# Optimization experiments

Measured on AMD Instinct MI355X. Metric: run time of the kernel, lower is better.

The kernel has to match this reference:

```python
import jax, jax.numpy as jnp
import numpy as np

NUM_FRAMES = 8
NUM_CLASSES = 40
INNER_TH = 0.5
MIN_WH = 0.05
SUPPRESS = 1e9


def _xyxy_to_cxcywh(b):
    x1, y1, x2, y2 = b[..., 0], b[..., 1], b[..., 2], b[..., 3]
    return jnp.stack([(x1 + x2) * 0.5, (y1 + y2) * 0.5, x2 - x1, y2 - y1], -1)


def setup_inputs() -> dict:
    key = jax.random.key(0)
    k1, k2, k3, k4, k5 = jax.random.split(key, 5)
    B, N, T = 4, 20, NUM_FRAMES
    H = W = 160
    # valid xyxy boxes: centers in [0.1,0.9], wh in [0.02,0.3]
    c = jax.random.uniform(k1, (B, N, T, 2), minval=0.1, maxval=0.9)
    wh = jax.random.uniform(k2, (B, N, T, 2), minval=0.02, maxval=0.3)
    gt_boxes = jnp.concatenate([c - wh / 2, c + wh / 2], -1).astype(jnp.float32)
    gt_labels = jax.random.randint(k3, (B, N), 0, NUM_CLASSES)
    ids = jax.random.randint(k4, (B, N, T), 0, 100)
    drop = jax.random.bernoulli(k5, 0.1, (B, N, T))
    gt_ids = jnp.where(drop, -1, ids)  # -1 => instance absent in that frame
    ys, xs = jnp.meshgrid(jnp.arange(H), jnp.arange(W), indexing='ij')
    ref_points = jnp.stack([(xs.reshape(-1) + 0.5) / W, (ys.reshape(-1) + 0.5) / H], -1).astype(jnp.float32)
    spatial_shapes = jnp.array([H, W], dtype=jnp.int32)
    return dict(gt_labels=gt_labels, gt_boxes=gt_boxes, gt_ids=gt_ids,
                ref_points=ref_points, spatial_shapes=spatial_shapes)


def _match_frame(dist_t, ids_t, labels, valid):
    # dist_t [N,P], ids_t [N], labels [N], valid [N]; sequential suppression over n
    N, P = dist_t.shape
    arangeP = jnp.arange(P)
    arangeC = jnp.arange(NUM_CLASSES)

    def step(carry, n):
        d_all, ml, md, mi = carry
        d = d_all[n]                                   # [P]
        act = valid[n] & (ids_t[n] != -1)
        inner = d < INNER_TH
        # if no inner point, claim just the single closest point
        pos = jnp.where(inner.any(), inner, arangeP == jnp.argmin(d)) & act
        lab = labels[n]
        score = 1.0 - 2.0 * jnp.clip(d, 0.0, INNER_TH)
        ml = jnp.where(pos, lab, ml)
        md = jnp.where(pos[:, None] & (arangeC == lab)[None, :], score[:, None], md)
        mi = jnp.where(pos, ids_t[n], mi)
        d_all = jnp.where(pos[None, :], SUPPRESS, d_all)  # suppress claimed points for all gts
        return (d_all, ml, md, mi), None

    init = (dist_t,
            jnp.full((P,), -1, jnp.int32),
            jnp.zeros((P, NUM_CLASSES), dist_t.dtype),
            jnp.full((P,), -1, jnp.int32))
    (_, ml, md, mi), _ = jax.lax.scan(step, init, jnp.arange(N))
    return ml, md, mi


def reference(gt_labels, gt_boxes, gt_ids, ref_points, spatial_shapes):
    B, N, T, _ = gt_boxes.shape
    boxes_c = _xyxy_to_cxcywh(gt_boxes)                 # [B,N,T,4]
    area = (boxes_c[..., 2] * boxes_c[..., 3]).mean(-1)  # [B,N] mean area over frames
    order = jnp.argsort(area, axis=1)                   # process small instances first
    boxes_c = jnp.take_along_axis(boxes_c, order[:, :, None, None], axis=1)
    labels = jnp.take_along_axis(gt_labels.astype(jnp.int32), order, axis=1)
    ids = jnp.take_along_axis(gt_ids.astype(jnp.int32), order[:, :, None], axis=1)
    valid = (boxes_c[..., 2:] > 0.0).all(-1).any(-1) & (labels >= 0)  # [B,N]
    # normalized center distance: [B,N,T,P]
    diff = (boxes_c[..., None, :2] - ref_points[None, None, None, :, :]) / jnp.clip(boxes_c[..., None, 2:], MIN_WH)
    dist = jnp.sum(diff ** 2, -1)
    f = jax.vmap(jax.vmap(_match_frame, in_axes=(1, 1, None, None)), in_axes=(0, 0, 0, 0))
    ml, md, mi = f(dist, ids, labels, valid)            # [B,T,P], [B,T,P,C], [B,T,P]
    return ml, md, mi
```

## Files before the change

kernel.cpp:

```cpp
#include <hip/hip_runtime.h>

#define BB   4
#define NGT  20
#define TT   8
#define PP   25600
#define CC   40
#define TPB  256
#define SUPP 1e9f
#define INNER_TH 0.5f
#define FILLB 224

#define PK_CLAIM  1u
#define PK_LAB_SH 1
#define PK_ID_SH  7
#define PK_MDV    (1u << 14)
#define PK_MDC_SH 15
#define PK_MDN_SH 21

__device__ inline unsigned long long shfl_down_u64(unsigned long long v, int off) {
    unsigned lo = (unsigned)v, hi = (unsigned)(v >> 32);
    lo = __shfl_down(lo, off, 64);
    hi = __shfl_down(hi, off, 64);
    return ((unsigned long long)hi << 32) | (unsigned long long)lo;
}

__device__ inline float4 make_geo(const float* __restrict__ gt_boxes, int b, int n, int t) {
    const float* bx = gt_boxes + ((size_t)(b * NGT + n) * TT + t) * 4;
    float x1 = bx[0], y1 = bx[1], x2 = bx[2], y2 = bx[3];
    float4 g;
    g.x = __fmul_rn(__fadd_rn(x1, x2), 0.5f);
    g.y = __fmul_rn(__fadd_rn(y1, y2), 0.5f);
    g.z = fmaxf(__fsub_rn(x2, x1), 0.05f);
    g.w = fmaxf(__fsub_rn(y2, y1), 0.05f);
    return g;
}

__device__ inline float point_dist(int px, int py, float4 g) {
    float rxv = __fdiv_rn((float)px + 0.5f, 160.0f);
    float ryv = __fdiv_rn((float)py + 0.5f, 160.0f);
    float dx = __fdiv_rn(__fsub_rn(g.x, rxv), g.z);
    float dy = __fdiv_rn(__fsub_rn(g.y, ryv), g.w);
    return __fadd_rn(__fmul_rn(dx, dx), __fmul_rn(dy, dy));
}

__global__ __launch_bounds__(TPB) void match_fill_kernel(
        const int*   __restrict__ gt_labels,
        const float* __restrict__ gt_boxes,
        const int*   __restrict__ gt_ids,
        unsigned* __restrict__ packs_g,
        uint4*    __restrict__ md4) {
    if (blockIdx.x >= BB * TT) {
        const int MD4 = BB * TT * PP * CC / 4;
        const int stride = FILLB * TPB;
        uint4 z = make_uint4(0u, 0u, 0u, 0u);
        for (int i = (blockIdx.x - BB * TT) * TPB + (int)threadIdx.x; i < MD4; i += stride)
            md4[i] = z;
        return;
    }

    int bt = blockIdx.x;
    int b  = bt >> 3;
    int t  = bt & 7;
    int tid = threadIdx.x;

    __shared__ unsigned s_pack[PP];
    __shared__ unsigned s_mask[160 * 5];
    __shared__ float  s_dxx[NGT * 160];
    __shared__ float  s_dyy[NGT * 160];
    __shared__ float  s_area[NGT];
    __shared__ int    s_valid[NGT];
    __shared__ int    s_order[NGT];
    __shared__ int    s_any[NGT];
    __shared__ float4 s_geo[NGT];
    __shared__ int4   s_meta[NGT];
    __shared__ int    s_actlist[NGT];
    __shared__ int    s_actcnt;
    __shared__ unsigned long long s_wave[TPB / 64];

    {
        uint4 z = make_uint4(0u, 0u, 0u, 0u);
        for (int i = tid; i < PP / 4; i += TPB) ((uint4*)s_pack)[i] = z;
        for (int i = tid; i < 160 * 5; i += TPB) s_mask[i] = 0u;
    }
    if (tid < NGT) {
        const float* bx = gt_boxes + (size_t)(b * NGT + tid) * TT * 4;
        float a[TT];
        int anyPos = 0;
        for (int f = 0; f < TT; f++) {
            float w = __fsub_rn(bx[f * 4 + 2], bx[f * 4 + 0]);
            float h = __fsub_rn(bx[f * 4 + 3], bx[f * 4 + 1]);
            a[f] = __fmul_rn(w, h);
            anyPos |= (w > 0.0f && h > 0.0f) ? 1 : 0;
        }
        float s = __fadd_rn(__fadd_rn(__fadd_rn(a[0], a[1]), __fadd_rn(a[2], a[3])),
                            __fadd_rn(__fadd_rn(a[4], a[5]), __fadd_rn(a[6], a[7])));
        s_area[tid]  = __fmul_rn(s, 0.125f);
        s_valid[tid] = (anyPos && gt_labels[b * NGT + tid] >= 0) ? 1 : 0;
        s_any[tid]   = 0;
    }
    __syncthreads();

    if (tid < NGT) {
        float an = s_area[tid];
        int r = 0;
        for (int m2 = 0; m2 < NGT; m2++) {
            float am = s_area[m2];
            r += (am < an || (am == an && m2 < tid)) ? 1 : 0;
        }
        s_order[r] = tid;
    }
    __syncthreads();

    if (tid < NGT) {
        int n   = s_order[tid];
        int src = b * NGT + n;
        s_geo[tid] = make_geo(gt_boxes, b, n, t);
        int id = gt_ids[src * TT + t];
        int4 mm;
        mm.x = gt_labels[src];
        mm.y = id;
        mm.z = (s_valid[n] && id != -1) ? 1 : 0;
        mm.w = n;
        s_meta[tid] = mm;
    }
    __syncthreads();
    if (tid == 0) {
        int c = 0;
        for (int k = 0; k < NGT; k++)
            if (s_meta[k].z) s_actlist[c++] = k;
        s_actcnt = c;
    }

    for (int i = tid; i < NGT * 320; i += TPB) {
        int slot = i / 320;
        int w    = i - slot * 320;
        float4 g = s_geo[slot];
        if (w < 160) {
            float rxv = __fdiv_rn((float)w + 0.5f, 160.0f);
            float dx  = __fdiv_rn(__fsub_rn(g.x, rxv), g.z);
            s_dxx[slot * 160 + w] = __fmul_rn(dx, dx);
        } else {
            int py = w - 160;
            float ryv = __fdiv_rn((float)py + 0.5f, 160.0f);
            float dy  = __fdiv_rn(__fsub_rn(g.y, ryv), g.w);
            s_dyy[slot * 160 + py] = __fmul_rn(dy, dy);
        }
    }
    __syncthreads();
    int actcnt = s_actcnt;

    for (int j = 0; j < actcnt; j++) {
        int slot = s_actlist[j];
        int4 m  = s_meta[slot];
        float4 g = s_geo[slot];
        const float* dxx = s_dxx + slot * 160;
        const float* dyy = s_dyy + slot * 160;

        float ex = __fmul_rn(g.z, 0.70711f);
        float ey = __fmul_rn(g.w, 0.70711f);
        int x0 = max(0,   (int)floorf((g.x - ex) * 160.0f - 0.5f) - 1);
        int x1 = min(159, (int)ceilf ((g.x + ex) * 160.0f - 0.5f) + 1);
        int y0 = max(0,   (int)floorf((g.y - ey) * 160.0f - 0.5f) - 1);
        int y1 = min(159, (int)ceilf ((g.y + ey) * 160.0f - 0.5f) + 1);
        int rw = x1 - x0 + 1;
        int M  = rw * (y1 - y0 + 1);

        unsigned base = PK_CLAIM | ((unsigned)m.x << PK_LAB_SH) |
                        ((unsigned)m.y << PK_ID_SH) | PK_MDV |
                        ((unsigned)m.x << PK_MDC_SH) |
                        ((unsigned)m.w << PK_MDN_SH);
        int found = 0;
        {
            int r  = tid / rw;
            int c  = tid - r * rw;
            int dr = TPB / rw;
            int dc = TPB - dr * rw;
            for (int i = tid; i < M; i += TPB) {
                int px = x0 + c;
                int py = y0 + r;
                int p  = py * 160 + px;
                if (!(s_pack[p] & PK_CLAIM)) {
                    float d = __fadd_rn(dxx[px], dyy[py]);
                    if (d < INNER_TH) {
                        s_pack[p] = base;
                        atomicOr(&s_mask[p >> 5], 1u << (p & 31));
                        found = 1;
                    }
                }
                c += dc; r += dr;
                if (c >= rw) { c -= rw; r++; }
            }
        }
        if (found) s_any[j] = 1;
        __syncthreads();

        if (!s_any[j]) {
            unsigned long long key = ~0ULL;
            if (tid < 160) {
                int y = tid;
                unsigned um[5];
#pragma unroll
                for (int w = 0; w < 5; w++) um[w] = ~s_mask[y * 5 + w];
                unsigned anyu = um[0] | um[1] | um[2] | um[3] | um[4];
                if (!anyu) {
                    if (y == 0)
                        key = ((unsigned long long)__float_as_uint(SUPP) << 32);
                } else {
                    float dyyv = dyy[y];
                    int xs = (int)floorf(__fsub_rn(__fmul_rn(g.x, 160.0f), 0.5f));
                    xs = min(max(xs, -2), 161);
                    float bd = 2e9f;
                    int   bx = -1;
#pragma unroll
                    for (int k2 = 0; k2 < 2; k2++) {
                        int x = xs + k2;
                        if (x >= 0 && x <= 159 && ((um[x >> 5] >> (x & 31)) & 1u)) {
                            float d2 = __fadd_rn(dxx[x], dyyv);
                            if (d2 < bd || (d2 == bd && x < bx)) { bd = d2; bx = x; }
                        }
                    }
                    {
                        int xq = min(xs - 1, 159);
                        int xL = -1;
                        if (xq >= 0) {
                            int w = xq >> 5;
                            unsigned mm = um[w] & (0xffffffffu >> (31 - (xq & 31)));
                            while (true) {
                                if (mm) { xL = (w << 5) + (31 - __clz(mm)); break; }
                                if (--w < 0) break;
                                mm = um[w];
                            }
                        }
                        if (xL >= 0) {
                            float dL = __fadd_rn(dxx[xL], dyyv);
                            while (xL > 0) {
                                int xq2 = xL - 1;
                                int w = xq2 >> 5;
                                unsigned mm = um[w] & (0xffffffffu >> (31 - (xq2 & 31)));
                                int x2 = -1;
                                while (true) {
                                    if (mm) { x2 = (w << 5) + (31 - __clz(mm)); break; }
                                    if (--w < 0) break;
                                    mm = um[w];
                                }
                                if (x2 < 0) break;
                                if (__fadd_rn(dxx[x2], dyyv) != dL) break;
                                xL = x2;
                            }
                            if (dL < bd || (dL == bd && xL < bx)) { bd = dL; bx = xL; }
                        }
                    }
                    {
                        int xq = max(xs + 2, 0);
                        int xR = -1;
                        if (xq <= 159) {
                            int w = xq >> 5;
                            unsigned mm = um[w] & (0xffffffffu << (xq & 31));
                            while (true) {
                                if (mm) { xR = (w << 5) + (__ffs(mm) - 1); break; }
                                if (++w > 4) break;
                                mm = um[w];
                            }
                        }
                        if (xR >= 0) {
                            float dR = __fadd_rn(dxx[xR], dyyv);
                            if (dR < bd || (dR == bd && xR < bx)) { bd = dR; bx = xR; }
                        }
                    }
                    if (bx >= 0) {
                        int p = y * 160 + bx;
                        key = ((unsigned long long)__float_as_uint(bd) << 32) |
                              (unsigned long long)(unsigned)p;
                    }
                }
            }
            unsigned long long v = key;
            for (int off = 32; off > 0; off >>= 1) {
                unsigned long long o = shfl_down_u64(v, off);
                v = (o < v) ? o : v;
            }
            int lane = tid & 63, wave = tid >> 6;
            if (lane == 0) s_wave[wave] = v;
            __syncthreads();
            if (tid == 0) {
                unsigned long long gmin = s_wave[0];
                for (int w = 1; w < TPB / 64; w++)
                    gmin = (s_wave[w] < gmin) ? s_wave[w] : gmin;
                float minv = __uint_as_float((unsigned)(gmin >> 32));
                int minp = (int)(unsigned)(gmin & 0xffffffffu);
                unsigned npk = PK_CLAIM | ((unsigned)m.x << PK_LAB_SH) |
                               ((unsigned)m.y << PK_ID_SH);
                if (minv < SUPP) {
                    s_pack[minp] = npk;
                } else {
                    unsigned old = s_pack[minp];
                    unsigned mdbits = old & (PK_MDV | (63u << PK_MDC_SH) | (31u << PK_MDN_SH));
                    if ((old & PK_MDV) &&
                        ((old >> PK_MDC_SH) & 63u) == (unsigned)m.x) mdbits = 0u;
                    s_pack[minp] = npk | mdbits;
                }
                s_mask[minp >> 5] |= 1u << (minp & 31);
            }
            __syncthreads();
        }
    }

    __syncthreads();
    uint4* dst = (uint4*)(packs_g + (size_t)bt * PP);
    for (int i = tid; i < PP / 4; i += TPB) dst[i] = ((const uint4*)s_pack)[i];
}

__global__ __launch_bounds__(256) void scatter_kernel(
        const unsigned* __restrict__ packs,
        const float*    __restrict__ gt_boxes,
        float* __restrict__ out) {
    const int    ML = BB * TT * PP;
    const size_t MD = (size_t)BB * TT * PP * CC;
    int f = blockIdx.x * 256 + threadIdx.x;
    uint4 pk4 = ((const uint4*)packs)[f];

    float4 vml, vmi;
    vml.x = (pk4.x & PK_CLAIM) ? (float)((pk4.x >> PK_LAB_SH) & 63u) : -1.0f;
    vml.y = (pk4.y & PK_CLAIM) ? (float)((pk4.y >> PK_LAB_SH) & 63u) : -1.0f;
    vml.z = (pk4.z & PK_CLAIM) ? (float)((pk4.z >> PK_LAB_SH) & 63u) : -1.0f;
    vml.w = (pk4.w & PK_CLAIM) ? (float)((pk4.w >> PK_LAB_SH) & 63u) : -1.0f;
    vmi.x = (pk4.x & PK_CLAIM) ? (float)((pk4.x >> PK_ID_SH) & 127u) : -1.0f;
    vmi.y = (pk4.y & PK_CLAIM) ? (float)((pk4.y >> PK_ID_SH) & 127u) : -1.0f;
    vmi.z = (pk4.z & PK_CLAIM) ? (float)((pk4.z >> PK_ID_SH) & 127u) : -1.0f;
    vmi.w = (pk4.w & PK_CLAIM) ? (float)((pk4.w >> PK_ID_SH) & 127u) : -1.0f;
    ((float4*)out)[f] = vml;
    ((float4*)(out + ML + MD))[f] = vmi;

    int pt0 = f << 2;
#pragma unroll
    for (int k = 0; k < 4; k++) {
        unsigned pk = (k == 0) ? pk4.x : (k == 1) ? pk4.y : (k == 2) ? pk4.z : pk4.w;
        if (pk & PK_MDV) {
            int pt  = pt0 + k;
            int cls = (int)((pk >> PK_MDC_SH) & 63u);
            int n   = (int)((pk >> PK_MDN_SH) & 31u);
            int bt  = pt / PP;
            int p   = pt - bt * PP;
            int py  = p / 160;
            int px  = p - py * 160;
            float4 g = make_geo(gt_boxes, bt >> 3, n, bt & 7);
            float d  = point_dist(px, py, g);
            out[ML + (size_t)pt * CC + cls] = __fsub_rn(1.0f, __fmul_rn(2.0f, d));
        }
    }
}

extern "C" void kernel_launch(void* const* d_in, const int* in_sizes, int n_in,
                              void* d_out, int out_size, void* d_ws, size_t ws_size,
                              hipStream_t stream) {
    const int*   gt_labels = (const int*)d_in[0];
    const float* gt_boxes  = (const float*)d_in[1];
    const int*   gt_ids    = (const int*)d_in[2];

    unsigned* packs = (unsigned*)d_ws;
    float*    outf  = (float*)d_out;

    match_fill_kernel<<<BB * TT + FILLB, TPB, 0, stream>>>(
        gt_labels, gt_boxes, gt_ids, packs,
        (uint4*)(outf + BB * TT * PP));

    scatter_kernel<<<(BB * TT * PP / 4) / 256, 256, 0, stream>>>(packs, gt_boxes, outf);
}
```

Measured before the change: 181.5 us.

## Replace sequential inner-point claiming with parallel atomicMin ownership and fallback pass

The serial per-GT claim loop, which needed a barrier after every ground truth, becomes a single parallel pass. Each in-range point takes the smallest slot index that has it inside its threshold via shared atomicMin. Per-slot claim counts come from ballots, and the closest-point fallback runs only for slots with zero claims, rebuilding the claimed mask from byte owners. The block grows to 1024 threads, and the label/id outputs are written directly from the matching kernel with byte-sized owner codes. The scatter kernel then only writes the score entries, which removes the packed word round-trip but adds a fallback-suppression special case.

```diff
diff --git a/kernel.cpp b/kernel.cpp
--- a/kernel.cpp
+++ b/kernel.cpp
@@ -5,17 +5,12 @@
 #define TT   8
 #define PP   25600
 #define CC   40
-#define TPB  256
+#define TPB  1024
 #define SUPP 1e9f
 #define INNER_TH 0.5f
 #define FILLB 224
-
-#define PK_CLAIM  1u
-#define PK_LAB_SH 1
-#define PK_ID_SH  7
-#define PK_MDV    (1u << 14)
-#define PK_MDC_SH 15
-#define PK_MDN_SH 21
+#define NONEC 63u
+#define FBF   64u
 
 __device__ inline unsigned long long shfl_down_u64(unsigned long long v, int off) {
     unsigned lo = (unsigned)v, hi = (unsigned)(v >> 32);
@@ -47,8 +42,11 @@
         const int*   __restrict__ gt_labels,
         const float* __restrict__ gt_boxes,
         const int*   __restrict__ gt_ids,
-        unsigned* __restrict__ packs_g,
-        uint4*    __restrict__ md4) {
+        unsigned char* __restrict__ cand_ws,
+        int2*          __restrict__ meta_ws,
+        unsigned char* __restrict__ supp_ws,
+        float*         __restrict__ out,
+        uint4*         __restrict__ md4) {
     if (blockIdx.x >= BB * TT) {
         const int MD4 = BB * TT * PP * CC / 4;
         const int stride = FILLB * TPB;
@@ -61,26 +59,28 @@
     int bt = blockIdx.x;
     int b  = bt >> 3;
     int t  = bt & 7;
-    int tid = threadIdx.x;
-
-    __shared__ unsigned s_pack[PP];
-    __shared__ unsigned s_mask[160 * 5];
+    int tid  = threadIdx.x;
+    int lane = tid & 63;
+
+    __shared__ unsigned      s_cand[PP];
+    __shared__ unsigned char s_candb[PP];
+    __shared__ unsigned      s_mask[160 * 5];
     __shared__ float  s_dxx[NGT * 160];
     __shared__ float  s_dyy[NGT * 160];
     __shared__ float  s_area[NGT];
     __shared__ int    s_valid[NGT];
     __shared__ int    s_order[NGT];
-    __shared__ int    s_any[NGT];
     __shared__ float4 s_geo[NGT];
     __shared__ int4   s_meta[NGT];
     __shared__ int    s_actlist[NGT];
     __shared__ int    s_actcnt;
+    __shared__ int    s_count[NGT];
     __shared__ unsigned long long s_wave[TPB / 64];
+    __shared__ unsigned s_suppmd;
 
     {
-        uint4 z = make_uint4(0u, 0u, 0u, 0u);
-        for (int i = tid; i < PP / 4; i += TPB) ((uint4*)s_pack)[i] = z;
-        for (int i = tid; i < 160 * 5; i += TPB) s_mask[i] = 0u;
+        uint4 ini = make_uint4(NONEC, NONEC, NONEC, NONEC);
+        for (int i = tid; i < PP / 4; i += TPB) ((uint4*)s_cand)[i] = ini;
     }
     if (tid < NGT) {
         const float* bx = gt_boxes + (size_t)(b * NGT + tid) * TT * 4;
@@ -96,8 +96,9 @@
                             __fadd_rn(__fadd_rn(a[4], a[5]), __fadd_rn(a[6], a[7])));
         s_area[tid]  = __fmul_rn(s, 0.125f);
         s_valid[tid] = (anyPos && gt_labels[b * NGT + tid] >= 0) ? 1 : 0;
-        s_any[tid]   = 0;
-    }
+        s_count[tid] = 0;
+    }
+    if (tid == 0) s_suppmd = 255u;
     __syncthreads();
 
     if (tid < NGT) {
@@ -149,13 +150,11 @@
     __syncthreads();
     int actcnt = s_actcnt;
 
-    for (int j = 0; j < actcnt; j++) {
-        int slot = s_actlist[j];
-        int4 m  = s_meta[slot];
+    for (int jj = 0; jj < actcnt; jj++) {
+        int slot = s_actlist[jj];
         float4 g = s_geo[slot];
         const float* dxx = s_dxx + slot * 160;
         const float* dyy = s_dyy + slot * 160;
-
         float ex = __fmul_rn(g.z, 0.70711f);
         float ey = __fmul_rn(g.w, 0.70711f);
         int x0 = max(0,   (int)floorf((g.x - ex) * 160.0f - 0.5f) - 1);
@@ -164,188 +163,230 @@
         int y1 = min(159, (int)ceilf ((g.y + ey) * 160.0f - 0.5f) + 1);
         int rw = x1 - x0 + 1;
         int M  = rw * (y1 - y0 + 1);
-
-        unsigned base = PK_CLAIM | ((unsigned)m.x << PK_LAB_SH) |
-                        ((unsigned)m.y << PK_ID_SH) | PK_MDV |
-                        ((unsigned)m.x << PK_MDC_SH) |
-                        ((unsigned)m.w << PK_MDN_SH);
-        int found = 0;
-        {
-            int r  = tid / rw;
-            int c  = tid - r * rw;
-            int dr = TPB / rw;
-            int dc = TPB - dr * rw;
-            for (int i = tid; i < M; i += TPB) {
-                int px = x0 + c;
-                int py = y0 + r;
-                int p  = py * 160 + px;
-                if (!(s_pack[p] & PK_CLAIM)) {
-                    float d = __fadd_rn(dxx[px], dyy[py]);
-                    if (d < INNER_TH) {
-                        s_pack[p] = base;
-                        atomicOr(&s_mask[p >> 5], 1u << (p & 31));
-                        found = 1;
+        int r  = tid / rw;
+        int c  = tid - r * rw;
+        int dr = TPB / rw;
+        int dc = TPB - dr * rw;
+        for (int i = tid; i < M; i += TPB) {
+            int px = x0 + c;
+            int py = y0 + r;
+            float d = __fadd_rn(dxx[px], dyy[py]);
+            if (d < INNER_TH) atomicMin(&s_cand[py * 160 + px], (unsigned)slot);
+            c += dc; r += dr;
+            if (c >= rw) { c -= rw; r++; }
+        }
+    }
+    __syncthreads();
+
+    {
+        unsigned lcnt = 0;
+        for (int i = tid; i < PP; i += TPB) {
+            unsigned cc = s_cand[i];
+            s_candb[i] = (unsigned char)cc;
+            for (int k = 0; k < NGT; k++) {
+                unsigned long long bl = __ballot(cc == (unsigned)k);
+                if (lane == k) lcnt += (unsigned)__popcll(bl);
+            }
+        }
+        if (lane < NGT) atomicAdd(&s_count[lane], (int)lcnt);
+    }
+    __syncthreads();
+
+    for (int jj = 0; jj < actcnt; jj++) {
+        int slot = s_actlist[jj];
+        if (s_count[slot] != 0) continue;
+
+        int4 m  = s_meta[slot];
+        float4 g = s_geo[slot];
+        const float* dxx = s_dxx + slot * 160;
+        const float* dyy = s_dyy + slot * 160;
+
+        for (int w = tid; w < 160 * 5; w += TPB) {
+            const unsigned* cw = ((const unsigned*)s_candb) + (w << 3);
+            unsigned mb = 0u;
+#pragma unroll
+            for (int q = 0; q < 8; q++) {
+                unsigned v = cw[q];
+                mb |= (((v        & 63u) < (unsigned)slot) ? 1u : 0u) << (q * 4 + 0);
+                mb |= ((((v >> 8)  & 63u) < (unsigned)slot) ? 1u : 0u) << (q * 4 + 1);
+                mb |= ((((v >> 16) & 63u) < (unsigned)slot) ? 1u : 0u) << (q * 4 + 2);
+                mb |= ((((v >> 24) & 63u) < (unsigned)slot) ? 1u : 0u) << (q * 4 + 3);
+            }
+            s_mask[w] = mb;
+        }
+        __syncthreads();
+
+        unsigned long long key = ~0ULL;
+        if (tid < 160) {
+            int y = tid;
+            unsigned um[5];
+#pragma unroll
+            for (int w = 0; w < 5; w++) um[w] = ~s_mask[y * 5 + w];
+            unsigned anyu = um[0] | um[1] | um[2] | um[3] | um[4];
+            if (!anyu) {
+                if (y == 0)
+                    key = ((unsigned long long)__float_as_uint(SUPP) << 32);
+            } else {
+                float dyyv = dyy[y];
+                int xs = (int)floorf(__fsub_rn(__fmul_rn(g.x, 160.0f), 0.5f));
+                xs = min(max(xs, -2), 161);
+                float bd = 2e9f;
+                int   bx = -1;
+#pragma unroll
+                for (int k2 = 0; k2 < 2; k2++) {
+                    int x = xs + k2;
+                    if (x >= 0 && x <= 159 && ((um[x >> 5] >> (x & 31)) & 1u)) {
+                        float d2 = __fadd_rn(dxx[x], dyyv);
+                        if (d2 < bd || (d2 == bd && x < bx)) { bd = d2; bx = x; }
                     }
                 }
-                c += dc; r += dr;
-                if (c >= rw) { c -= rw; r++; }
-            }
-        }
-        if (found) s_any[j] = 1;
-        __syncthreads();
-
-        if (!s_any[j]) {
-            unsigned long long key = ~0ULL;
-            if (tid < 160) {
-                int y = tid;
-                unsigned um[5];
-#pragma unroll
-                for (int w = 0; w < 5; w++) um[w] = ~s_mask[y * 5 + w];
-                unsigned anyu = um[0] | um[1] | um[2] | um[3] | um[4];
-                if (!anyu) {
-                    if (y == 0)
-                        key = ((unsigned long long)__float_as_uint(SUPP) << 32);
-                } else {
-                    float dyyv = dyy[y];
-                    int xs = (int)floorf(__fsub_rn(__fmul_rn(g.x, 160.0f), 0.5f));
-                    xs = min(max(xs, -2), 161);
-                    float bd = 2e9f;
-                    int   bx = -1;
-#pragma unroll
-                    for (int k2 = 0; k2 < 2; k2++) {
-                        int x = xs + k2;
-                        if (x >= 0 && x <= 159 && ((um[x >> 5] >> (x & 31)) & 1u)) {
-                            float d2 = __fadd_rn(dxx[x], dyyv);
-                            if (d2 < bd || (d2 == bd && x < bx)) { bd = d2; bx = x; }
+                {
+                    int xq = min(xs - 1, 159);
+                    int xL = -1;
+                    if (xq >= 0) {
+                        int w = xq >> 5;
+                        unsigned mm = um[w] & (0xffffffffu >> (31 - (xq & 31)));
+                        while (true) {
+                            if (mm) { xL = (w << 5) + (31 - __clz(mm)); break; }
+                            if (--w < 0) break;
+                            mm = um[w];
                         }
                     }
-                    {
-                        int xq = min(xs - 1, 159);
-                        int xL = -1;
-                        if (xq >= 0) {
-                            int w = xq >> 5;
-                            unsigned mm = um[w] & (0xffffffffu >> (31 - (xq & 31)));
+                    if (xL >= 0) {
+                        float dL = __fadd_rn(dxx[xL], dyyv);
+                        while (xL > 0) {
+                            int xq2 = xL - 1;
+                            int w = xq2 >> 5;
+                            unsigned mm = um[w] & (0xffffffffu >> (31 - (xq2 & 31)));
+                            int x2 = -1;
                             while (true) {
-                                if (mm) { xL = (w << 5) + (31 - __clz(mm)); break; }
+                                if (mm) { x2 = (w << 5) + (31 - __clz(mm)); break; }
                                 if (--w < 0) break;
                                 mm = um[w];
                             }
+                            if (x2 < 0) break;
+                            if (__fadd_rn(dxx[x2], dyyv) != dL) break;
+                            xL = x2;
                         }
-                        if (xL >= 0) {
-                            float dL = __fadd_rn(dxx[xL], dyyv);
-                            while (xL > 0) {
-                                int xq2 = xL - 1;
-                                int w = xq2 >> 5;
-                                unsigned mm = um[w] & (0xffffffffu >> (31 - (xq2 & 31)));
-                                int x2 = -1;
-                                while (true) {
-                                    if (mm) { x2 = (w << 5) + (31 - __clz(mm)); break; }
-                                    if (--w < 0) break;
-                                    mm = um[w];
-                                }
-                                if (x2 < 0) break;
-                                if (__fadd_rn(dxx[x2], dyyv) != dL) break;
-                                xL = x2;
-                            }
-                            if (dL < bd || (dL == bd && xL < bx)) { bd = dL; bx = xL; }
+                        if (dL < bd || (dL == bd && xL < bx)) { bd = dL; bx = xL; }
+                    }
+                }
+                {
+                    int xq = max(xs + 2, 0);
+                    int xR = -1;
+                    if (xq <= 159) {
+                        int w = xq >> 5;
+                        unsigned mm = um[w] & (0xffffffffu << (xq & 31));
+                        while (true) {
+                            if (mm) { xR = (w << 5) + (__ffs(mm) - 1); break; }
+                            if (++w > 4) break;
+                            mm = um[w];
                         }
                     }
-                    {
-                        int xq = max(xs + 2, 0);
-                        int xR = -1;
-                        if (xq <= 159) {
-                            int w = xq >> 5;
-                            unsigned mm = um[w] & (0xffffffffu << (xq & 31));
-                            while (true) {
-                                if (mm) { xR = (w << 5) + (__ffs(mm) - 1); break; }
-                                if (++w > 4) break;
-                                mm = um[w];
-                            }
-                        }
-                        if (xR >= 0) {
-                            float dR = __fadd_rn(dxx[xR], dyyv);
-                            if (dR < bd || (dR == bd && xR < bx)) { bd = dR; bx = xR; }
-                        }
-                    }
-                    if (bx >= 0) {
-                        int p = y * 160 + bx;
-                        key = ((unsigned long long)__float_as_uint(bd) << 32) |
-                              (unsigned long long)(unsigned)p;
+                    if (xR >= 0) {
+                        float dR = __fadd_rn(dxx[xR], dyyv);
+                        if (dR < bd || (dR == bd && xR < bx)) { bd = dR; bx = xR; }
                     }
                 }
+                if (bx >= 0) {
+                    int p = y * 160 + bx;
+                    key = ((unsigned long long)__float_as_uint(bd) << 32) |
+                          (unsigned long long)(unsigned)p;
+                }
             }
-            unsigned long long v = key;
-            for (int off = 32; off > 0; off >>= 1) {
-                unsigned long long o = shfl_down_u64(v, off);
-                v = (o < v) ? o : v;
+        }
+        unsigned long long v = key;
+        for (int off = 32; off > 0; off >>= 1) {
+            unsigned long long o = shfl_down_u64(v, off);
+            v = (o < v) ? o : v;
+        }
+        if (lane == 0) s_wave[tid >> 6] = v;
+        __syncthreads();
+        if (tid == 0) {
+            unsigned long long gmin = s_wave[0];
+            for (int w = 1; w < TPB / 64; w++)
+                gmin = (s_wave[w] < gmin) ? s_wave[w] : gmin;
+            float minv = __uint_as_float((unsigned)(gmin >> 32));
+            int minp = (int)(unsigned)(gmin & 0xffffffffu);
+            if (minv < SUPP) {
+                unsigned old = s_candb[minp];
+                if (old != NONEC) s_count[old]--;
+                s_candb[minp] = (unsigned char)((unsigned)slot | FBF);
+            } else {
+                unsigned old = s_candb[0];
+                unsigned curmd = (old & FBF) ? s_suppmd :
+                                 ((old != NONEC) ? (unsigned)old : 255u);
+                if (curmd != 255u && s_meta[curmd & 63u].x == m.x) curmd = 255u;
+                s_suppmd = curmd;
+                s_candb[0] = (unsigned char)((unsigned)slot | FBF);
             }
-            int lane = tid & 63, wave = tid >> 6;
-            if (lane == 0) s_wave[wave] = v;
-            __syncthreads();
-            if (tid == 0) {
-                unsigned long long gmin = s_wave[0];
-                for (int w = 1; w < TPB / 64; w++)
-                    gmin = (s_wave[w] < gmin) ? s_wave[w] : gmin;
-                float minv = __uint_as_float((unsigned)(gmin >> 32));
-                int minp = (int)(unsigned)(gmin & 0xffffffffu);
-                unsigned npk = PK_CLAIM | ((unsigned)m.x << PK_LAB_SH) |
-                               ((unsigned)m.y << PK_ID_SH);
-                if (minv < SUPP) {
-                    s_pack[minp] = npk;
-                } else {
-                    unsigned old = s_pack[minp];
-                    unsigned mdbits = old & (PK_MDV | (63u << PK_MDC_SH) | (31u << PK_MDN_SH));
-                    if ((old & PK_MDV) &&
-                        ((old >> PK_MDC_SH) & 63u) == (unsigned)m.x) mdbits = 0u;
-                    s_pack[minp] = npk | mdbits;
-                }
-                s_mask[minp >> 5] |= 1u << (minp & 31);
+        }
+        __syncthreads();
+    }
+
+    const int MDOFF4 = (BB * TT * PP + BB * TT * PP * CC) / 4;
+    float4* out4 = (float4*)out;
+    for (int i = tid; i < PP / 4; i += TPB) {
+        unsigned cw = ((const unsigned*)s_candb)[i];
+        float4 vml, vmi;
+#pragma unroll
+        for (int k = 0; k < 4; k++) {
+            unsigned c = (cw >> (8 * k)) & 255u;
+            float ml, mi;
+            if (c == NONEC) { ml = -1.0f; mi = -1.0f; }
+            else {
+                int s = (int)(c & 63u);
+                ml = (float)s_meta[s].x;
+                mi = (float)s_meta[s].y;
             }
-            __syncthreads();
-        }
-    }
-
-    __syncthreads();
-    uint4* dst = (uint4*)(packs_g + (size_t)bt * PP);
-    for (int i = tid; i < PP / 4; i += TPB) dst[i] = ((const uint4*)s_pack)[i];
-}
-
-__global__ __launch_bounds__(256) void scatter_kernel(
-        const unsigned* __restrict__ packs,
-        const float*    __restrict__ gt_boxes,
+            ((float*)&vml)[k] = ml;
+            ((float*)&vmi)[k] = mi;
+        }
+        out4[bt * (PP / 4) + i] = vml;
+        out4[MDOFF4 + bt * (PP / 4) + i] = vmi;
+    }
+    for (int i = tid; i < PP / 16; i += TPB)
+        ((uint4*)(cand_ws + (size_t)bt * PP))[i] = ((const uint4*)s_candb)[i];
+    if (tid < NGT) {
+        int4 mm = s_meta[tid];
+        meta_ws[bt * NGT + tid] = make_int2(mm.x, mm.w);
+    }
+    if (tid == 0) supp_ws[bt] = (unsigned char)s_suppmd;
+}
+
+__global__ __launch_bounds__(256) void md_scatter_kernel(
+        const unsigned char* __restrict__ cand_ws,
+        const int2*          __restrict__ meta_ws,
+        const unsigned char* __restrict__ supp_ws,
+        const float*         __restrict__ gt_boxes,
         float* __restrict__ out) {
-    const int    ML = BB * TT * PP;
-    const size_t MD = (size_t)BB * TT * PP * CC;
-    int f = blockIdx.x * 256 + threadIdx.x;
-    uint4 pk4 = ((const uint4*)packs)[f];
-
-    float4 vml, vmi;
-    vml.x = (pk4.x & PK_CLAIM) ? (float)((pk4.x >> PK_LAB_SH) & 63u) : -1.0f;
-    vml.y = (pk4.y & PK_CLAIM) ? (float)((pk4.y >> PK_LAB_SH) & 63u) : -1.0f;
-    vml.z = (pk4.z & PK_CLAIM) ? (float)((pk4.z >> PK_LAB_SH) & 63u) : -1.0f;
-    vml.w = (pk4.w & PK_CLAIM) ? (float)((pk4.w >> PK_LAB_SH) & 63u) : -1.0f;
-    vmi.x = (pk4.x & PK_CLAIM) ? (float)((pk4.x >> PK_ID_SH) & 127u) : -1.0f;
-    vmi.y = (pk4.y & PK_CLAIM) ? (float)((pk4.y >> PK_ID_SH) & 127u) : -1.0f;
-    vmi.z = (pk4.z & PK_CLAIM) ? (float)((pk4.z >> PK_ID_SH) & 127u) : -1.0f;
-    vmi.w = (pk4.w & PK_CLAIM) ? (float)((pk4.w >> PK_ID_SH) & 127u) : -1.0f;
-    ((float4*)out)[f] = vml;
-    ((float4*)(out + ML + MD))[f] = vmi;
-
-    int pt0 = f << 2;
+    const int ML = BB * TT * PP;
+    int f4 = blockIdx.x * 256 + threadIdx.x;
+    unsigned cw = ((const unsigned*)cand_ws)[f4];
+    int pt0 = f4 << 2;
 #pragma unroll
     for (int k = 0; k < 4; k++) {
-        unsigned pk = (k == 0) ? pk4.x : (k == 1) ? pk4.y : (k == 2) ? pk4.z : pk4.w;
-        if (pk & PK_MDV) {
-            int pt  = pt0 + k;
-            int cls = (int)((pk >> PK_MDC_SH) & 63u);
-            int n   = (int)((pk >> PK_MDN_SH) & 31u);
-            int bt  = pt / PP;
-            int p   = pt - bt * PP;
-            int py  = p / 160;
-            int px  = p - py * 160;
-            float4 g = make_geo(gt_boxes, bt >> 3, n, bt & 7);
-            float d  = point_dist(px, py, g);
-            out[ML + (size_t)pt * CC + cls] = __fsub_rn(1.0f, __fmul_rn(2.0f, d));
+        unsigned c = (cw >> (8 * k)) & 255u;
+        if (c != NONEC && !(c & FBF)) {
+            int pt = pt0 + k;
+            int bt = pt / PP;
+            int p  = pt - bt * PP;
+            int2 mr = meta_ws[bt * NGT + (int)c];
+            float4 g = make_geo(gt_boxes, bt >> 3, mr.y, bt & 7);
+            int py = p / 160;
+            int px = p - py * 160;
+            float d = point_dist(px, py, g);
+            out[ML + (size_t)pt * CC + mr.x] = __fsub_rn(1.0f, __fmul_rn(2.0f, d));
+        }
+    }
+    if (f4 % (PP / 4) == 0) {
+        int bt = f4 / (PP / 4);
+        unsigned sm = supp_ws[bt];
+        if (sm != 255u) {
+            int2 mr = meta_ws[bt * NGT + (int)(sm & 63u)];
+            float4 g = make_geo(gt_boxes, bt >> 3, mr.y, bt & 7);
+            float d = point_dist(0, 0, g);
+            out[ML + (size_t)bt * PP * CC + mr.x] = __fsub_rn(1.0f, __fmul_rn(2.0f, d));
         }
     }
 }
@@ -357,12 +398,15 @@
     const float* gt_boxes  = (const float*)d_in[1];
     const int*   gt_ids    = (const int*)d_in[2];
 
-    unsigned* packs = (unsigned*)d_ws;
-    float*    outf  = (float*)d_out;
+    unsigned char* cand_ws = (unsigned char*)d_ws;
+    int2*          meta_ws = (int2*)((char*)d_ws + BB * TT * PP);
+    unsigned char* supp_ws = (unsigned char*)d_ws + BB * TT * PP + BB * TT * NGT * 8;
+    float*         outf    = (float*)d_out;
 
     match_fill_kernel<<<BB * TT + FILLB, TPB, 0, stream>>>(
-        gt_labels, gt_boxes, gt_ids, packs,
+        gt_labels, gt_boxes, gt_ids, cand_ws, meta_ws, supp_ws, outf,
         (uint4*)(outf + BB * TT * PP));
 
-    scatter_kernel<<<(BB * TT * PP / 4) / 256, 256, 0, stream>>>(packs, gt_boxes, outf);
-}
+    md_scatter_kernel<<<(BB * TT * PP / 4) / 256, 256, 0, stream>>>(
+        cand_ws, meta_ws, supp_ws, gt_boxes, outf);
+}
```

New measurement: 170.1 us. -6.3%, faster.
